# Kernel tuning notes

Hardware: AMD Instinct MI355X
Metric: run time of the kernel (lower is better)

The kernel has to match this reference:

```python
import jax, jax.numpy as jnp
import numpy as np

T = 500_000  # sequence length
K = 16       # number of hidden states


def setup_inputs() -> dict:
    key = jax.random.key(0)
    k1, k2, k3, k4 = jax.random.split(key, 4)
    y = jax.random.normal(k1, (T,), dtype=jnp.float32)
    transition_logits = jax.random.normal(k2, (K, K), dtype=jnp.float32)
    mu = 2.0 * jax.random.normal(k3, (K,), dtype=jnp.float32)
    log_sigma = 0.1 * jax.random.normal(k4, (K,), dtype=jnp.float32)
    return {"y": y, "transition_logits": transition_logits, "mu": mu, "log_sigma": log_sigma}


def _stationary_distribution(P):
    # Solve pi P = pi, sum(pi) = 1 via least squares (normal equations: differentiable, jit-safe).
    k = P.shape[0]
    A = jnp.concatenate([P.T - jnp.eye(k, dtype=P.dtype), jnp.ones((1, k), dtype=P.dtype)], axis=0)
    b = jnp.concatenate([jnp.zeros((k,), dtype=P.dtype), jnp.ones((1,), dtype=P.dtype)])
    return jnp.linalg.solve(A.T @ A, A.T @ b)


def reference(y, transition_logits, mu, log_sigma):
    P = jax.nn.softmax(transition_logits, axis=-1)  # [K, K] row-stochastic transition matrix
    sigma = jnp.exp(log_sigma)
    # Gaussian emission densities g[t, k] = N(y_t; mu_k, sigma_k^2)
    z = (y[:, None] - mu[None, :]) / sigma[None, :]
    INV_SQRT_2PI = 0.3989422804014327
    g = jnp.exp(-0.5 * z * z) * (INV_SQRT_2PI / sigma)[None, :]  # [T, K]

    ut0 = _stationary_distribution(P)              # [K]
    g0 = g[0]
    ft0 = jnp.sum(ut0 * g0)                        # scalar
    utt0 = ut0 * g0 / ft0                          # [K]

    def step(utt_prev, gt):
        ut = utt_prev @ P                          # predictive dist [K]
        ft = jnp.sum(ut * gt)                      # normalizer
        utt = ut * gt / ft                         # filtered posterior [K]
        return utt, (ut, ft, utt)

    _, (Ut, ft_rest, Utt) = jax.lax.scan(step, utt0, g[1:])

    ut = jnp.concatenate([ut0[None, :], Ut], axis=0)       # [T, K]
    u_norm = jnp.concatenate([utt0[None, :], Utt], axis=0)  # [T, K]
    ft = jnp.concatenate([ft0[None], ft_rest], axis=0)      # [T]
    return (ut, u_norm, ft)
```

## Files before the change

kernel.cpp:

```cpp
#include <hip/hip_runtime.h>

#define CHUNK_L 16
#define WARMUP_W 32

template<int K> __device__ __forceinline__ float bcast16(float v) {
    return __int_as_float(__builtin_amdgcn_update_dpp(
        0, __float_as_int(v), 0x150 | K, 0xF, 0xF, true));
}
template<int N> __device__ __forceinline__ float rowror16(float v) {
    return __int_as_float(__builtin_amdgcn_update_dpp(
        0, __float_as_int(v), 0x120 | N, 0xF, 0xF, true));
}

__device__ __forceinline__ float dot16(float a, const float* pc) {
    float u0 = bcast16<0>(a)  * pc[0];
    float u1 = bcast16<1>(a)  * pc[1];
    float u2 = bcast16<2>(a)  * pc[2];
    float u3 = bcast16<3>(a)  * pc[3];
    u0 = fmaf(bcast16<4>(a),  pc[4],  u0);
    u1 = fmaf(bcast16<5>(a),  pc[5],  u1);
    u2 = fmaf(bcast16<6>(a),  pc[6],  u2);
    u3 = fmaf(bcast16<7>(a),  pc[7],  u3);
    u0 = fmaf(bcast16<8>(a),  pc[8],  u0);
    u1 = fmaf(bcast16<9>(a),  pc[9],  u1);
    u2 = fmaf(bcast16<10>(a), pc[10], u2);
    u3 = fmaf(bcast16<11>(a), pc[11], u3);
    u0 = fmaf(bcast16<12>(a), pc[12], u0);
    u1 = fmaf(bcast16<13>(a), pc[13], u1);
    u2 = fmaf(bcast16<14>(a), pc[14], u2);
    u3 = fmaf(bcast16<15>(a), pc[15], u3);
    return (u0 + u1) + (u2 + u3);
}

__device__ __forceinline__ float rowsum16(float p) {
    p += rowror16<1>(p);
    p += rowror16<2>(p);
    p += rowror16<4>(p);
    p += rowror16<8>(p);
    return p;
}

__global__ __launch_bounds__(256, 8) void hmm_filter_kernel(
    const float* __restrict__ y,
    const float* __restrict__ logits,
    const float* __restrict__ mu,
    const float* __restrict__ log_sigma,
    float* __restrict__ out,
    int T, int nchunks)
{
    __shared__ float Plds[256];
    __shared__ float Ba[256];
    __shared__ float Bb[256];

    const int tid = (int)threadIdx.x;
    const int j   = tid & 15;
    const int g   = tid >> 4;

    float l = logits[tid];
    float m = l;
    #pragma unroll
    for (int s = 1; s < 16; s <<= 1) m = fmaxf(m, __shfl_xor(m, s, 16));
    float e = __expf(l - m);
    float rs = e;
    #pragma unroll
    for (int s = 1; s < 16; s <<= 1) rs += __shfl_xor(rs, s, 16);
    float Pv = e / rs;
    Plds[tid] = Pv;
    Ba[tid]   = Pv;
    __syncthreads();

    float* cur = Ba;
    float* nxt = Bb;
    for (int itq = 0; itq < 10; ++itq) {
        float acc = 0.f;
        #pragma unroll
        for (int k = 0; k < 16; ++k)
            acc += cur[g * 16 + k] * cur[k * 16 + j];
        float rsum = acc;
        #pragma unroll
        for (int s = 1; s < 16; s <<= 1) rsum += __shfl_xor(rsum, s, 16);
        nxt[tid] = acc / rsum;
        __syncthreads();
        float* tmp = cur; cur = nxt; nxt = tmp;
    }

    const float api = cur[j];

    float pc[16];
    #pragma unroll
    for (int k = 0; k < 16; ++k) pc[k] = Plds[k * 16 + j];

    const float muj = mu[j];
    const float isj = __expf(-log_sigma[j]);
    const float nmj = -muj * isj;
    const float lcf = __log2f(0.3989422804014327f * isj);
    const float K2  = -0.7213475204444817f;

    const int chunk = (int)blockIdx.x * 16 + g;
    if (chunk >= nchunks) return;

    const int wfrom = chunk * CHUNK_L;
    int t0 = wfrom - WARMUP_W; if (t0 < 0) t0 = 0;
    const int nwb = (wfrom - t0) >> 2;
    const int Tm4 = T - 4;
    const int TN  = T << 4;

    float a = api;

    auto wstep = [&](float av, float yt) -> float {
        float up = dot16(av, pc);
        float z  = fmaf(yt, isj, nmj);
        float gj = __builtin_amdgcn_exp2f(fmaf(z * z, K2, lcf));
        return up * gj;
    };
    auto mstep = [&](float av, float yt, int off, float& sOut) -> float {
        float up = dot16(av, pc);
        float z  = fmaf(yt, isj, nmj);
        float gj = __builtin_amdgcn_exp2f(fmaf(z * z, K2, lcf));
        float p  = up * gj;
        float s  = rowsum16(p);
        float an = p * __builtin_amdgcn_rcpf(s);
        out[off]      = up;
        out[TN + off] = an;
        sOut = s;
        return an;
    };

    int t = t0;
    float4 c4 = *(const float4*)(y + t);
    int p1 = t + 4; if (p1 > Tm4) p1 = Tm4;
    float4 n1 = *(const float4*)(y + p1);

    for (int b = 0; b < nwb; ++b) {
        int p2 = t + 8; if (p2 > Tm4) p2 = Tm4;
        const float4 n2 = *(const float4*)(y + p2);
        a = wstep(a, c4.x);
        a = wstep(a, c4.y);
        a = wstep(a, c4.z);
        a = wstep(a, c4.w);
        if (b & 1) a *= __builtin_amdgcn_rcpf(rowsum16(a));
        c4 = n1; n1 = n2; t += 4;
    }
    a *= __builtin_amdgcn_rcpf(rowsum16(a));

    int oU = (wfrom << 4) + j;
    #pragma unroll 1
    for (int b = 0; b < (CHUNK_L / 4); ++b) {
        int p2 = t + 8; if (p2 > Tm4) p2 = Tm4;
        const float4 n2 = *(const float4*)(y + p2);
        float s0, s1, s2, s3;
        a = mstep(a, c4.x, oU +  0, s0);
        a = mstep(a, c4.y, oU + 16, s1);
        a = mstep(a, c4.z, oU + 32, s2);
        a = mstep(a, c4.w, oU + 48, s3);
        if (j == 0)
            *(float4*)(out + 2 * TN + t) = make_float4(s0, s1, s2, s3);
        c4 = n1; n1 = n2; t += 4; oU += 64;
    }
}

extern "C" void kernel_launch(void* const* d_in, const int* in_sizes, int n_in,
                              void* d_out, int out_size, void* d_ws, size_t ws_size,
                              hipStream_t stream) {
    const float* y      = (const float*)d_in[0];
    const float* logits = (const float*)d_in[1];
    const float* mu     = (const float*)d_in[2];
    const float* ls     = (const float*)d_in[3];
    float* out = (float*)d_out;
    const int T = in_sizes[0];

    const int nchunks = (T + CHUNK_L - 1) / CHUNK_L;
    const int blocks  = (nchunks + 15) / 16;
    hmm_filter_kernel<<<blocks, 256, 0, stream>>>(y, logits, mu, ls, out,
                                                  T, nchunks);
}
```

Baseline: 108.8 us.

## Use packed FMA dot product, defer normalization off the chain, rebalance chunk/warmup

Rewrites the 16-term predictive dot product with 2-wide float vectors so the compiler can emit packed FMA instructions. In the main loop the per-step normalization is taken off the serial dependency chain: unnormalized products are propagated and the reciprocal of each row sum is applied afterwards to the stored outputs. Chunk length doubles and warmup halves, which cuts redundant warmup work, and warmup renormalizes only once. The launch-bounds occupancy hint drops from 8 to 4. Risks are a less converged filter start from the shorter warmup and possible overflow or underflow from unnormalized propagation over four steps.

```diff
diff --git a/kernel.cpp b/kernel.cpp
--- a/kernel.cpp
+++ b/kernel.cpp
@@ -1,7 +1,9 @@
 #include <hip/hip_runtime.h>
 
-#define CHUNK_L 16
-#define WARMUP_W 32
+#define CHUNK_L 32
+#define WARMUP_W 16
+
+typedef float v2f __attribute__((ext_vector_type(2)));
 
 template<int K> __device__ __forceinline__ float bcast16(float v) {
     return __int_as_float(__builtin_amdgcn_update_dpp(
@@ -12,26 +14,6 @@
         0, __float_as_int(v), 0x120 | N, 0xF, 0xF, true));
 }
 
-__device__ __forceinline__ float dot16(float a, const float* pc) {
-    float u0 = bcast16<0>(a)  * pc[0];
-    float u1 = bcast16<1>(a)  * pc[1];
-    float u2 = bcast16<2>(a)  * pc[2];
-    float u3 = bcast16<3>(a)  * pc[3];
-    u0 = fmaf(bcast16<4>(a),  pc[4],  u0);
-    u1 = fmaf(bcast16<5>(a),  pc[5],  u1);
-    u2 = fmaf(bcast16<6>(a),  pc[6],  u2);
-    u3 = fmaf(bcast16<7>(a),  pc[7],  u3);
-    u0 = fmaf(bcast16<8>(a),  pc[8],  u0);
-    u1 = fmaf(bcast16<9>(a),  pc[9],  u1);
-    u2 = fmaf(bcast16<10>(a), pc[10], u2);
-    u3 = fmaf(bcast16<11>(a), pc[11], u3);
-    u0 = fmaf(bcast16<12>(a), pc[12], u0);
-    u1 = fmaf(bcast16<13>(a), pc[13], u1);
-    u2 = fmaf(bcast16<14>(a), pc[14], u2);
-    u3 = fmaf(bcast16<15>(a), pc[15], u3);
-    return (u0 + u1) + (u2 + u3);
-}
-
 __device__ __forceinline__ float rowsum16(float p) {
     p += rowror16<1>(p);
     p += rowror16<2>(p);
@@ -40,7 +22,29 @@
     return p;
 }
 
-__global__ __launch_bounds__(256, 8) void hmm_filter_kernel(
+__device__ __forceinline__ float dot16(float a, const v2f* pc2) {
+    v2f b0, b1, u01, u23;
+    b0.x = bcast16<0>(a);  b0.y = bcast16<1>(a);
+    b1.x = bcast16<2>(a);  b1.y = bcast16<3>(a);
+    u01 = b0 * pc2[0];
+    u23 = b1 * pc2[1];
+    b0.x = bcast16<4>(a);  b0.y = bcast16<5>(a);
+    b1.x = bcast16<6>(a);  b1.y = bcast16<7>(a);
+    u01 = b0 * pc2[2] + u01;
+    u23 = b1 * pc2[3] + u23;
+    b0.x = bcast16<8>(a);  b0.y = bcast16<9>(a);
+    b1.x = bcast16<10>(a); b1.y = bcast16<11>(a);
+    u01 = b0 * pc2[4] + u01;
+    u23 = b1 * pc2[5] + u23;
+    b0.x = bcast16<12>(a); b0.y = bcast16<13>(a);
+    b1.x = bcast16<14>(a); b1.y = bcast16<15>(a);
+    u01 = b0 * pc2[6] + u01;
+    u23 = b1 * pc2[7] + u23;
+    v2f u = u01 + u23;
+    return u.x + u.y;
+}
+
+__global__ __launch_bounds__(256, 4) void hmm_filter_kernel(
     const float* __restrict__ y,
     const float* __restrict__ logits,
     const float* __restrict__ mu,
@@ -86,9 +90,12 @@
 
     const float api = cur[j];
 
-    float pc[16];
+    v2f pc2[8];
     #pragma unroll
-    for (int k = 0; k < 16; ++k) pc[k] = Plds[k * 16 + j];
+    for (int k = 0; k < 8; ++k) {
+        pc2[k].x = Plds[(2 * k)     * 16 + j];
+        pc2[k].y = Plds[(2 * k + 1) * 16 + j];
+    }
 
     const float muj = mu[j];
     const float isj = __expf(-log_sigma[j]);
@@ -105,57 +112,71 @@
     const int Tm4 = T - 4;
     const int TN  = T << 4;
 
-    float a = api;
-
-    auto wstep = [&](float av, float yt) -> float {
-        float up = dot16(av, pc);
-        float z  = fmaf(yt, isj, nmj);
-        float gj = __builtin_amdgcn_exp2f(fmaf(z * z, K2, lcf));
-        return up * gj;
-    };
-    auto mstep = [&](float av, float yt, int off, float& sOut) -> float {
-        float up = dot16(av, pc);
-        float z  = fmaf(yt, isj, nmj);
-        float gj = __builtin_amdgcn_exp2f(fmaf(z * z, K2, lcf));
-        float p  = up * gj;
-        float s  = rowsum16(p);
-        float an = p * __builtin_amdgcn_rcpf(s);
-        out[off]      = up;
-        out[TN + off] = an;
-        sOut = s;
-        return an;
+    auto emis = [&](float yt) -> float {
+        float z = fmaf(yt, isj, nmj);
+        return __builtin_amdgcn_exp2f(fmaf(z * z, K2, lcf));
     };
 
+    float p = api;
     int t = t0;
+
     float4 c4 = *(const float4*)(y + t);
-    int p1 = t + 4; if (p1 > Tm4) p1 = Tm4;
-    float4 n1 = *(const float4*)(y + p1);
+    int pf = t + 4; if (pf > Tm4) pf = Tm4;
+    float4 n1 = *(const float4*)(y + pf);
 
     for (int b = 0; b < nwb; ++b) {
         int p2 = t + 8; if (p2 > Tm4) p2 = Tm4;
         const float4 n2 = *(const float4*)(y + p2);
-        a = wstep(a, c4.x);
-        a = wstep(a, c4.y);
-        a = wstep(a, c4.z);
-        a = wstep(a, c4.w);
-        if (b & 1) a *= __builtin_amdgcn_rcpf(rowsum16(a));
+        p = dot16(p, pc2) * emis(c4.x);
+        p = dot16(p, pc2) * emis(c4.y);
+        p = dot16(p, pc2) * emis(c4.z);
+        p = dot16(p, pc2) * emis(c4.w);
+        if (b == 1) p *= __builtin_amdgcn_rcpf(rowsum16(p));
         c4 = n1; n1 = n2; t += 4;
     }
-    a *= __builtin_amdgcn_rcpf(rowsum16(a));
+    p *= __builtin_amdgcn_rcpf(rowsum16(p));
 
-    int oU = (wfrom << 4) + j;
+    float* __restrict__ pU = out + (wfrom << 4) + j;
+    float* __restrict__ pN = pU + TN;
+    float* __restrict__ pF = out + 2 * TN + wfrom;
+
     #pragma unroll 1
     for (int b = 0; b < (CHUNK_L / 4); ++b) {
         int p2 = t + 8; if (p2 > Tm4) p2 = Tm4;
         const float4 n2 = *(const float4*)(y + p2);
-        float s0, s1, s2, s3;
-        a = mstep(a, c4.x, oU +  0, s0);
-        a = mstep(a, c4.y, oU + 16, s1);
-        a = mstep(a, c4.z, oU + 32, s2);
-        a = mstep(a, c4.w, oU + 48, s3);
+
+        const float q0  = dot16(p, pc2);
+        const float pg0 = q0 * emis(c4.x);
+        const float s0  = rowsum16(pg0);
+        const float r0  = __builtin_amdgcn_rcpf(s0);
+        const float q1  = dot16(pg0, pc2);
+        const float pg1 = q1 * emis(c4.y);
+        const float s1  = rowsum16(pg1);
+        const float r1  = __builtin_amdgcn_rcpf(s1);
+        const float q2  = dot16(pg1, pc2);
+        const float pg2 = q2 * emis(c4.z);
+        const float s2  = rowsum16(pg2);
+        const float r2  = __builtin_amdgcn_rcpf(s2);
+        const float q3  = dot16(pg2, pc2);
+        const float pg3 = q3 * emis(c4.w);
+        const float s3  = rowsum16(pg3);
+        const float r3  = __builtin_amdgcn_rcpf(s3);
+
+        pU[0]  = q0;
+        pU[16] = q1 * r0;
+        pU[32] = q2 * r1;
+        pU[48] = q3 * r2;
+        pN[0]  = pg0 * r0;
+        pN[16] = pg1 * r1;
+        pN[32] = pg2 * r2;
+        const float utt3 = pg3 * r3;
+        pN[48] = utt3;
         if (j == 0)
-            *(float4*)(out + 2 * TN + t) = make_float4(s0, s1, s2, s3);
-        c4 = n1; n1 = n2; t += 4; oU += 64;
+            *(float4*)pF = make_float4(s0, s1 * r0, s2 * r1, s3 * r2);
+
+        p = utt3;
+        pU += 64; pN += 64; pF += 4;
+        c4 = n1; n1 = n2; t += 4;
     }
 }
 
```

After: 95.44 us. -12.3%, faster.
